# Optimization experiments

Hardware: AMD Instinct MI355X
Metric: run time of the kernel (lower is better)

## Reference

```python
import jax, jax.numpy as jnp
import numpy as np

B, S, D = 2, 2048, 1024
H, Hd = 16, 64
THD = H * Hd  # total_head_dim
LAMBDA_INIT = 0.8
ROPE_BASE = 10000.0
GN_EPS = 1e-5


def _rope_tables(seq_len, head_dim, dtype):
    inv_freq = 1.0 / (ROPE_BASE ** (jnp.arange(0, head_dim, 2, dtype=jnp.float32) / head_dim))
    t = jnp.arange(seq_len, dtype=jnp.float32)
    freqs = jnp.outer(t, inv_freq)                      # (S, Hd/2)
    emb = jnp.concatenate([freqs, freqs], axis=-1)      # (S, Hd)
    return jnp.cos(emb).astype(dtype), jnp.sin(emb).astype(dtype)


def _rotate_half(x):
    x1, x2 = jnp.split(x, 2, axis=-1)
    return jnp.concatenate([-x2, x1], axis=-1)


def _apply_rope(q, k, cos, sin):
    # q, k: (B, H, S, Hd); cos/sin: (S, Hd)
    cos = cos[None, None, :, :]
    sin = sin[None, None, :, :]
    q = q * cos + _rotate_half(q) * sin
    k = k * cos + _rotate_half(k) * sin
    return q, k


def setup_inputs() -> dict:
    key = jax.random.key(0)
    ks = jax.random.split(key, 8)
    s_in = 1.0 / np.sqrt(D)
    s_out = 1.0 / np.sqrt(THD)
    return {
        "x": jax.random.normal(ks[0], (B, S, D), dtype=jnp.float32),
        "Wq": jax.random.normal(ks[1], (D, 2 * THD), dtype=jnp.float32) * s_in,
        "Wk": jax.random.normal(ks[2], (D, 2 * THD), dtype=jnp.float32) * s_in,
        "Wv": jax.random.normal(ks[3], (D, THD), dtype=jnp.float32) * s_in,
        "Wo": jax.random.normal(ks[4], (THD, D), dtype=jnp.float32) * s_out,
        "lambda_q1": jnp.full((H,), LAMBDA_INIT, dtype=jnp.float32),
        "lambda_k1": jnp.full((H,), LAMBDA_INIT, dtype=jnp.float32),
        "lambda_q2": jnp.full((H,), LAMBDA_INIT, dtype=jnp.float32),
        "lambda_k2": jnp.full((H,), LAMBDA_INIT, dtype=jnp.float32),
        "lambda_init": jnp.asarray(LAMBDA_INIT, dtype=jnp.float32),
        "gn_weight": jnp.ones((THD,), dtype=jnp.float32),
        "gn_bias": jnp.zeros((THD,), dtype=jnp.float32),
    }


def reference(x, Wq, Wk, Wv, Wo, lambda_q1, lambda_k1, lambda_q2, lambda_k2,
              lambda_init, gn_weight, gn_bias):
    b, s, _ = x.shape
    scale = Hd ** -0.5

    q = (x @ Wq).reshape(b, s, 2, H, Hd).transpose(0, 2, 3, 1, 4)  # (B,2,H,S,Hd)
    k = (x @ Wk).reshape(b, s, 2, H, Hd).transpose(0, 2, 3, 1, 4)
    v = (x @ Wv).reshape(b, s, H, Hd).transpose(0, 2, 1, 3)        # (B,H,S,Hd)

    q1, q2 = q[:, 0], q[:, 1]
    k1, k2 = k[:, 0], k[:, 1]

    cos, sin = _rope_tables(s, Hd, x.dtype)
    q1, k1 = _apply_rope(q1, k1, cos, sin)
    q2, k2 = _apply_rope(q2, k2, cos, sin)

    attn1 = jax.nn.softmax(jnp.einsum("bhqd,bhkd->bhqk", q1, k1) * scale, axis=-1)
    attn2 = jax.nn.softmax(jnp.einsum("bhqd,bhkd->bhqk", q2, k2) * scale, axis=-1)

    lam1 = jnp.exp(lambda_q1 * lambda_k1).reshape(1, H, 1, 1)
    lam2 = jnp.exp(lambda_q2 * lambda_k2).reshape(1, H, 1, 1)
    lam_full = lam1 - lam2 + lambda_init

    attn_diff = attn1 - lam_full * attn2
    out = jnp.einsum("bhqk,bhkd->bhqd", attn_diff, v)              # (B,H,S,Hd)
    out = out.transpose(0, 2, 1, 3).reshape(b * s, H, Hd)           # (B*S,H,Hd)

    # GroupNorm with num_groups=H over channels THD: normalize each head's Hd
    mean = out.mean(axis=-1, keepdims=True)
    var = out.var(axis=-1, keepdims=True)
    out = (out - mean) * jax.lax.rsqrt(var + GN_EPS)
    out = out * gn_weight.reshape(H, Hd) + gn_bias.reshape(H, Hd)

    out = out.reshape(b, s, THD) * (1.0 - lambda_init)
    return out @ Wo
```

## Files before the change

kernel.cpp:

```cpp
#include <hip/hip_runtime.h>
#include <hip/hip_fp16.h>
#include <math.h>

#define NH     16
#define HD     64
#define S_LEN  2048
#define THD_   1024
#define SCALE_LOG2E 0.18033688011112042f

typedef __fp16 f16x8 __attribute__((ext_vector_type(8)));
typedef __fp16 f16x4 __attribute__((ext_vector_type(4)));
typedef __fp16 f16x2 __attribute__((ext_vector_type(2)));
typedef float  f32x4 __attribute__((ext_vector_type(4)));


__device__ inline void wt_body(const float* __restrict__ W,
                               __half* __restrict__ WT, int id, int nmask,
                               int nshift) {
  int n = id & nmask;
  int k8 = (id >> nshift) * 8;
  int N = nmask + 1;
  f16x8 h;
#pragma unroll
  for (int j = 0; j < 8; ++j)
    h[j] = (__fp16)W[(size_t)(k8 + j) * N + n];
  *(f16x8*)(WT + (size_t)n * 1024 + k8) = h;
}

__global__ __launch_bounds__(256) void prep_kernel(
    const float* __restrict__ Wq, const float* __restrict__ Wk,
    __half* __restrict__ WqT, __half* __restrict__ WkT,
    float2* __restrict__ tab) {
  int bid = blockIdx.x;
  int t = threadIdx.x;
  if (bid < 1024) {
    wt_body(Wq, WqT, bid * 256 + t, 2047, 11);
  } else if (bid < 2048) {
    wt_body(Wk, WkT, (bid - 1024) * 256 + t, 2047, 11);
  } else {
    int id = (bid - 2048) * 256 + t;
    int p = id & 31;
    int s = id >> 5;
    float inv = expf(-0.28782313662425574f * (float)p);
    float sn, cs;
    sincosf((float)s * inv, &sn, &cs);
    tab[id] = make_float2(cs, sn);
  }
}

template <int MODE>
__global__ __launch_bounds__(256) void mfma_gemm(const void* __restrict__ Ap,
                                                 const void* __restrict__ Bp,
                                                 void* __restrict__ Cp,
                                                 const float2* __restrict__ tab) {
  __shared__ __fp16 As[128][72];
  __shared__ __fp16 Bs[64][72];
  const int t = threadIdx.x;
  const int w = t >> 6, lane = t & 63;
  const int quad = lane >> 4, lqi = lane & 15;
  const int wm = w * 32;
  const int n0 = blockIdx.x * 64, m0 = blockIdx.y * 128;

  f32x4 acc[2][4];
#pragma unroll
  for (int mt = 0; mt < 2; ++mt)
#pragma unroll
    for (int nt = 0; nt < 4; ++nt) acc[mt][nt] = (f32x4){0.f, 0.f, 0.f, 0.f};

  const int srow = t >> 3;
  const int sc8 = (t & 7) * 8;
  const int gn_ = t & 63;
  const int gk0 = (t >> 6) * 8;

  for (int k0 = 0; k0 < 1024; k0 += 64) {
    if (k0) __syncthreads();
    if (MODE == 3) {
      const __half* A16 = (const __half*)Ap;
#pragma unroll
      for (int p = 0; p < 4; ++p) {
        int row = srow + 32 * p;
        *(f16x8*)&As[row][sc8] =
            *(const f16x8*)(A16 + (size_t)(m0 + row) * 1024 + k0 + sc8);
      }
    } else {
      const float* A32 = (const float*)Ap;
#pragma unroll
      for (int p = 0; p < 4; ++p) {
        int row = srow + 32 * p;
        const float* src = A32 + (size_t)(m0 + row) * 1024 + k0 + sc8;
        float4 u = *(const float4*)src;
        float4 v = *(const float4*)(src + 4);
        f16x8 h;
        h[0] = (__fp16)u.x; h[1] = (__fp16)u.y;
        h[2] = (__fp16)u.z; h[3] = (__fp16)u.w;
        h[4] = (__fp16)v.x; h[5] = (__fp16)v.y;
        h[6] = (__fp16)v.z; h[7] = (__fp16)v.w;
        *(f16x8*)&As[row][sc8] = h;
      }
    }
    if (MODE == 2) {
      const float* B32 = (const float*)Bp;
#pragma unroll
      for (int p = 0; p < 2; ++p) {
        int kc = gk0 + 32 * p;
        f16x8 h;
#pragma unroll
        for (int j = 0; j < 8; ++j)
          h[j] = (__fp16)B32[(size_t)(k0 + kc + j) * 1024 + n0 + gn_];
        *(f16x8*)&Bs[gn_][kc] = h;
      }
    } else {
      const __half* B16 = (const __half*)Bp;
      if (srow < 32) {
#pragma unroll
        for (int p = 0; p < 2; ++p) {
          int row = srow + 32 * p;
          *(f16x8*)&Bs[row][sc8] =
              *(const f16x8*)(B16 + (size_t)(n0 + row) * 1024 + k0 + sc8);
        }
      }
    }
    __syncthreads();
#pragma unroll
    for (int ks = 0; ks < 2; ++ks) {
      f16x8 af[2], bf[4];
#pragma unroll
      for (int mt = 0; mt < 2; ++mt)
        af[mt] = *(const f16x8*)&As[wm + mt * 16 + lqi][ks * 32 + quad * 8];
#pragma unroll
      for (int nt = 0; nt < 4; ++nt)
        bf[nt] = *(const f16x8*)&Bs[nt * 16 + lqi][ks * 32 + quad * 8];
#pragma unroll
      for (int mt = 0; mt < 2; ++mt)
#pragma unroll
        for (int nt = 0; nt < 4; ++nt)
          acc[mt][nt] = __builtin_amdgcn_mfma_f32_16x16x32_f16(
              af[mt], bf[nt], acc[mt][nt], 0, 0, 0);
    }
  }

  const int b = m0 >> 11;
  const int s0 = (m0 & 2047) + wm + quad * 4;
  if (MODE == 0) {
    __half* dst = (__half*)Cp;
    const int comp = n0 >> 10, hh = (n0 >> 6) & 15;
    __half* base = dst + ((size_t)(b * 2 + comp) * NH + hh) * (size_t)S_LEN * HD;
#pragma unroll
    for (int nt = 0; nt < 2; ++nt) {
      int p = nt * 16 + lqi;
#pragma unroll
      for (int mt = 0; mt < 2; ++mt) {
#pragma unroll
        for (int i = 0; i < 4; ++i) {
          int s = s0 + mt * 16 + i;
          float2 cs = tab[s * 32 + p];
          float x1 = acc[mt][nt][i], x2 = acc[mt][nt + 2][i];
          base[(size_t)s * HD + p] = __float2half(x1 * cs.x - x2 * cs.y);
          base[(size_t)s * HD + p + 32] = __float2half(x2 * cs.x + x1 * cs.y);
        }
      }
    }
  } else if (MODE == 2) {
    __half* vt = (__half*)Cp;
    const int hh = n0 >> 6;
#pragma unroll
    for (int nt = 0; nt < 4; ++nt) {
      int hd = nt * 16 + lqi;
      __half* base = vt + (((size_t)b * NH + hh) * HD + hd) * S_LEN;
#pragma unroll
      for (int mt = 0; mt < 2; ++mt) {
        f16x4 hv;
#pragma unroll
        for (int i = 0; i < 4; ++i) hv[i] = (__fp16)acc[mt][nt][i];
        *(f16x4*)(base + s0 + mt * 16) = hv;
      }
    }
  } else {
    float* Co = (float*)Cp;
#pragma unroll
    for (int mt = 0; mt < 2; ++mt)
#pragma unroll
      for (int i = 0; i < 4; ++i) {
        int m = m0 + wm + mt * 16 + quad * 4 + i;
#pragma unroll
        for (int nt = 0; nt < 4; ++nt)
          Co[(size_t)m * 1024 + n0 + nt * 16 + lqi] = acc[mt][nt][i];
      }
  }
}

__global__ __launch_bounds__(256, 2) void attn_kernel(
    const __half* __restrict__ q_h, const __half* __restrict__ k_h,
    const __half* __restrict__ vt_h, float* __restrict__ out,
    const float* __restrict__ lq1, const float* __restrict__ lk1,
    const float* __restrict__ lq2, const float* __restrict__ lk2,
    const float* __restrict__ lam_init_p) {
  __shared__ __half KV[24][512];
  __shared__ __half P_lds[4][2][32][72];

  const int t = threadIdx.x;
  const int w = t >> 6, lane = t & 63;
  const int quad = lane >> 4, lqi = lane & 15;
  const int qt = blockIdx.x;
  const int bh = blockIdx.y;
  const int b = bh >> 4, h = bh & 15;

  const size_t c1 = ((size_t)(b * 2 + 0) * NH + h) * (size_t)S_LEN * HD;
  const size_t c2 = ((size_t)(b * 2 + 1) * NH + h) * (size_t)S_LEN * HD;
  const size_t vtb = ((size_t)b * NH + h) * (size_t)HD * S_LEN;
  const int q0 = qt * 128 + w * 32;

  f16x8 qf[2][2][2];
#pragma unroll
  for (int nt = 0; nt < 2; ++nt)
#pragma unroll
    for (int ks = 0; ks < 2; ++ks) {
      size_t a = (size_t)(q0 + nt * 16 + lqi) * HD + ks * 32 + quad * 8;
      qf[0][nt][ks] = *(const f16x8*)(q_h + c1 + a);
      qf[1][nt][ks] = *(const f16x8*)(q_h + c2 + a);
    }

  f32x4 O[2][4][2];
#pragma unroll
  for (int s = 0; s < 2; ++s)
#pragma unroll
    for (int mt = 0; mt < 4; ++mt)
#pragma unroll
      for (int nt = 0; nt < 2; ++nt) O[s][mt][nt] = (f32x4){0.f, 0.f, 0.f, 0.f};
  float lsum[2][2] = {{0.f, 0.f}, {0.f, 0.f}};

  auto chunk_addr = [&](int c, int k0) -> const __half* {
    if (c < 16) {
      int str = c >> 3, mt = (c >> 1) & 3, ks = c & 1;
      return k_h + (str ? c2 : c1) + (size_t)(k0 + mt * 16 + lqi) * HD +
             ks * 32 + quad * 8;
    }
    int cc = c - 16, ks2 = cc >> 2, mt = cc & 3;
    return vt_h + vtb + (size_t)(mt * 16 + lqi) * S_LEN + k0 + ks2 * 32 +
           quad * 8;
  };

  f16x8 r[6];
#pragma unroll
  for (int ci = 0; ci < 6; ++ci)
    r[ci] = *(const f16x8*)chunk_addr(w + ci * 4, 0);

  for (int kt = 0; kt < 32; ++kt) {
    if (kt) __syncthreads();
#pragma unroll
    for (int ci = 0; ci < 6; ++ci)
      *(f16x8*)&KV[w + ci * 4][lane * 8] = r[ci];
    __syncthreads();

    if (kt < 31) {
#pragma unroll
      for (int ci = 0; ci < 6; ++ci)
        r[ci] = *(const f16x8*)chunk_addr(w + ci * 4, (kt + 1) * 64);
    }

#pragma unroll
    for (int mt = 0; mt < 4; ++mt) {
#pragma unroll
      for (int str = 0; str < 2; ++str) {
        f16x8 kf0 = *(const f16x8*)&KV[str * 8 + mt * 2 + 0][lane * 8];
        f16x8 kf1 = *(const f16x8*)&KV[str * 8 + mt * 2 + 1][lane * 8];
#pragma unroll
        for (int nt = 0; nt < 2; ++nt) {
          f32x4 s = (f32x4){0.f, 0.f, 0.f, 0.f};
          s = __builtin_amdgcn_mfma_f32_16x16x32_f16(kf0, qf[str][nt][0], s,
                                                     0, 0, 0);
          s = __builtin_amdgcn_mfma_f32_16x16x32_f16(kf1, qf[str][nt][1], s,
                                                     0, 0, 0);
          float e0 = __builtin_amdgcn_exp2f(s[0] * SCALE_LOG2E);
          float e1 = __builtin_amdgcn_exp2f(s[1] * SCALE_LOG2E);
          float e2 = __builtin_amdgcn_exp2f(s[2] * SCALE_LOG2E);
          float e3 = __builtin_amdgcn_exp2f(s[3] * SCALE_LOG2E);
          lsum[str][nt] += (e0 + e1) + (e2 + e3);
          union { f16x4 v; f16x2 h2[2]; } pu;
          pu.h2[0] = __builtin_amdgcn_cvt_pkrtz(e0, e1);
          pu.h2[1] = __builtin_amdgcn_cvt_pkrtz(e2, e3);
          *(f16x4*)&P_lds[w][str][nt * 16 + lqi][mt * 16 + quad * 4] = pu.v;
        }
      }
    }
#pragma unroll
    for (int ks2 = 0; ks2 < 2; ++ks2) {
      f16x8 pf[2][2];
#pragma unroll
      for (int str = 0; str < 2; ++str)
#pragma unroll
        for (int nt = 0; nt < 2; ++nt)
          pf[str][nt] = *(const f16x8*)&P_lds[w][str][nt * 16 + lqi]
                                             [ks2 * 32 + quad * 8];
#pragma unroll
      for (int mt = 0; mt < 4; ++mt) {
        f16x8 vf = *(const f16x8*)&KV[16 + ks2 * 4 + mt][lane * 8];
#pragma unroll
        for (int str = 0; str < 2; ++str)
#pragma unroll
          for (int nt = 0; nt < 2; ++nt)
            O[str][mt][nt] = __builtin_amdgcn_mfma_f32_16x16x32_f16(
                vf, pf[str][nt], O[str][mt][nt], 0, 0, 0);
      }
    }
  }

  const float lam0 = lam_init_p[0];
  const float lam = expf(lq1[h] * lk1[h]) - expf(lq2[h] * lk2[h]) + lam0;
#pragma unroll
  for (int str = 0; str < 2; ++str)
#pragma unroll
    for (int nt = 0; nt < 2; ++nt) {
      float v = lsum[str][nt];
      v += __shfl_xor(v, 16);
      v += __shfl_xor(v, 32);
      lsum[str][nt] = v;
    }
#pragma unroll
  for (int nt = 0; nt < 2; ++nt) {
    float il1 = 1.f / lsum[0][nt];
    float il2 = lam / lsum[1][nt];
    int q = q0 + nt * 16 + lqi;
#pragma unroll
    for (int mt = 0; mt < 4; ++mt) {
      f32x4 o;
#pragma unroll
      for (int i = 0; i < 4; ++i)
        o[i] = O[0][mt][nt][i] * il1 - O[1][mt][nt][i] * il2;
      *(f32x4*)(out + ((size_t)(b * S_LEN + q)) * THD_ + h * HD + mt * 16 +
                quad * 4) = o;
    }
  }
}

__global__ __launch_bounds__(256) void gn_wt_kernel(
    const float* __restrict__ src, __half* __restrict__ dst,
    const float* __restrict__ gw, const float* __restrict__ gb,
    const float* __restrict__ lam_init_p, const float* __restrict__ Wo,
    __half* __restrict__ WoT) {
  if (blockIdx.x >= 16384) {
    wt_body(Wo, WoT, (blockIdx.x - 16384) * 256 + threadIdx.x, 1023, 10);
    return;
  }
  int g = blockIdx.x * 4 + (threadIdx.x >> 6);
  int lane = threadIdx.x & 63;
  float v = src[(size_t)g * 64 + lane];
  float s = v, sq = v * v;
#pragma unroll
  for (int off = 32; off; off >>= 1) {
    s += __shfl_xor(s, off);
    sq += __shfl_xor(sq, off);
  }
  float mean = s * (1.f / 64.f);
  float var = sq * (1.f / 64.f) - mean * mean;
  float rs = rsqrtf(var + 1e-5f);
  int h = g & 15;
  float w = gw[h * 64 + lane], bb = gb[h * 64 + lane];
  dst[(size_t)g * 64 + lane] =
      __float2half(((v - mean) * rs * w + bb) * (1.f - lam_init_p[0]));
}

extern "C" void kernel_launch(void* const* d_in, const int* in_sizes, int n_in,
                              void* d_out, int out_size, void* d_ws,
                              size_t ws_size, hipStream_t stream) {
  const float* x = (const float*)d_in[0];
  const float* Wq = (const float*)d_in[1];
  const float* Wk = (const float*)d_in[2];
  const float* Wv = (const float*)d_in[3];
  const float* Wo = (const float*)d_in[4];
  const float* lq1 = (const float*)d_in[5];
  const float* lk1 = (const float*)d_in[6];
  const float* lq2 = (const float*)d_in[7];
  const float* lk2 = (const float*)d_in[8];
  const float* lam_init = (const float*)d_in[9];
  const float* gnw = (const float*)d_in[10];
  const float* gnb = (const float*)d_in[11];
  float* out = (float*)d_out;

  __half* q_h = (__half*)d_ws;
  __half* k_h = q_h + 8388608;
  __half* vt_h = k_h + 8388608;
  __half* WqT = k_h;
  __half* WkT = vt_h;
  float2* tab = (float2*)(vt_h + 2097152);
  __half* WoT = q_h;
  __half* gn_h = q_h + 1048576;

  dim3 blk(256);
  prep_kernel<<<2304, blk, 0, stream>>>(Wq, Wk, WqT, WkT, tab);
  mfma_gemm<0><<<dim3(32, 32), blk, 0, stream>>>(x, WqT, q_h, tab);
  mfma_gemm<0><<<dim3(32, 32), blk, 0, stream>>>(x, WkT, k_h, tab);
  mfma_gemm<2><<<dim3(16, 32), blk, 0, stream>>>(x, Wv, vt_h, nullptr);
  attn_kernel<<<dim3(16, 32), blk, 0, stream>>>(q_h, k_h, vt_h, out, lq1, lk1,
                                                lq2, lk2, lam_init);
  gn_wt_kernel<<<16896, blk, 0, stream>>>(out, gn_h, gnw, gnb, lam_init, Wo,
                                          WoT);
  mfma_gemm<3><<<dim3(16, 32), blk, 0, stream>>>(gn_h, WoT, out, nullptr);
}
```

Before: 333.2 us.

## Keep softmax probabilities in registers, double-buffer K/V LDS, fold scale into Q

The attention kernel now feeds the exponentiated scores straight from the QK^T MFMA output registers into 16x16x16 MFMAs against V. This removes the per-warp P round trip through shared memory. K/V tiles are double-buffered in LDS with a re-laid-out V buffer, so there is one barrier per tile instead of two. The softmax scale times log2(e) is folded into Q when the Q projection is written, dropping a multiply per score, at the cost of rounding the scaled Q to fp16 and using smaller-K MFMAs.

```diff
diff --git a/kernel.cpp b/kernel.cpp
--- a/kernel.cpp
+++ b/kernel.cpp
@@ -141,7 +141,7 @@
 
   const int b = m0 >> 11;
   const int s0 = (m0 & 2047) + wm + quad * 4;
-  if (MODE == 0) {
+  if (MODE == 0 || MODE == 1) {
     __half* dst = (__half*)Cp;
     const int comp = n0 >> 10, hh = (n0 >> 6) & 15;
     __half* base = dst + ((size_t)(b * 2 + comp) * NH + hh) * (size_t)S_LEN * HD;
@@ -155,8 +155,11 @@
           int s = s0 + mt * 16 + i;
           float2 cs = tab[s * 32 + p];
           float x1 = acc[mt][nt][i], x2 = acc[mt][nt + 2][i];
-          base[(size_t)s * HD + p] = __float2half(x1 * cs.x - x2 * cs.y);
-          base[(size_t)s * HD + p + 32] = __float2half(x2 * cs.x + x1 * cs.y);
+          float y1 = x1 * cs.x - x2 * cs.y;
+          float y2 = x2 * cs.x + x1 * cs.y;
+          if (MODE == 1) { y1 *= SCALE_LOG2E; y2 *= SCALE_LOG2E; }
+          base[(size_t)s * HD + p] = __float2half(y1);
+          base[(size_t)s * HD + p + 32] = __float2half(y2);
         }
       }
     }
@@ -195,8 +198,8 @@
     const float* __restrict__ lq1, const float* __restrict__ lk1,
     const float* __restrict__ lq2, const float* __restrict__ lk2,
     const float* __restrict__ lam_init_p) {
-  __shared__ __half KV[24][512];
-  __shared__ __half P_lds[4][2][32][72];
+  __shared__ __half Ks[2][16][512];
+  __shared__ __half Vs[2][4][64][16];
 
   const int t = threadIdx.x;
   const int w = t >> 6, lane = t & 63;
@@ -224,12 +227,12 @@
 #pragma unroll
   for (int s = 0; s < 2; ++s)
 #pragma unroll
-    for (int mt = 0; mt < 4; ++mt)
-#pragma unroll
-      for (int nt = 0; nt < 2; ++nt) O[s][mt][nt] = (f32x4){0.f, 0.f, 0.f, 0.f};
+    for (int hm = 0; hm < 4; ++hm)
+#pragma unroll
+      for (int nt = 0; nt < 2; ++nt) O[s][hm][nt] = (f32x4){0.f, 0.f, 0.f, 0.f};
   float lsum[2][2] = {{0.f, 0.f}, {0.f, 0.f}};
 
-  auto chunk_addr = [&](int c, int k0) -> const __half* {
+  auto k_src = [&](int c, int k0) -> const __half* {
     if (c < 16) {
       int str = c >> 3, mt = (c >> 1) & 3, ks = c & 1;
       return k_h + (str ? c2 : c1) + (size_t)(k0 + mt * 16 + lqi) * HD +
@@ -239,31 +242,38 @@
     return vt_h + vtb + (size_t)(mt * 16 + lqi) * S_LEN + k0 + ks2 * 32 +
            quad * 8;
   };
+  auto lds_dst = [&](int c, int buf) -> __half* {
+    if (c < 16) return &Ks[buf][c][lane * 8];
+    int cc = c - 16, ks2 = cc >> 2, mt = cc & 3;
+    int kc = ks2 * 2 + (quad >> 1);
+    return &Vs[buf][kc][mt * 16 + lqi][(quad & 1) * 8];
+  };
 
   f16x8 r[6];
 #pragma unroll
-  for (int ci = 0; ci < 6; ++ci)
-    r[ci] = *(const f16x8*)chunk_addr(w + ci * 4, 0);
+  for (int ci = 0; ci < 6; ++ci) r[ci] = *(const f16x8*)k_src(w + ci * 4, 0);
+#pragma unroll
+  for (int ci = 0; ci < 6; ++ci) *(f16x8*)lds_dst(w + ci * 4, 0) = r[ci];
+  __syncthreads();
 
   for (int kt = 0; kt < 32; ++kt) {
-    if (kt) __syncthreads();
-#pragma unroll
-    for (int ci = 0; ci < 6; ++ci)
-      *(f16x8*)&KV[w + ci * 4][lane * 8] = r[ci];
-    __syncthreads();
-
+    const int cur = kt & 1;
     if (kt < 31) {
 #pragma unroll
       for (int ci = 0; ci < 6; ++ci)
-        r[ci] = *(const f16x8*)chunk_addr(w + ci * 4, (kt + 1) * 64);
+        r[ci] = *(const f16x8*)k_src(w + ci * 4, (kt + 1) * 64);
     }
 
 #pragma unroll
     for (int mt = 0; mt < 4; ++mt) {
+      f16x4 vf[4];
+#pragma unroll
+      for (int hm = 0; hm < 4; ++hm)
+        vf[hm] = *(const f16x4*)&Vs[cur][mt][hm * 16 + lqi][quad * 4];
 #pragma unroll
       for (int str = 0; str < 2; ++str) {
-        f16x8 kf0 = *(const f16x8*)&KV[str * 8 + mt * 2 + 0][lane * 8];
-        f16x8 kf1 = *(const f16x8*)&KV[str * 8 + mt * 2 + 1][lane * 8];
+        f16x8 kf0 = *(const f16x8*)&Ks[cur][str * 8 + mt * 2 + 0][lane * 8];
+        f16x8 kf1 = *(const f16x8*)&Ks[cur][str * 8 + mt * 2 + 1][lane * 8];
 #pragma unroll
         for (int nt = 0; nt < 2; ++nt) {
           f32x4 s = (f32x4){0.f, 0.f, 0.f, 0.f};
@@ -271,37 +281,27 @@
                                                      0, 0, 0);
           s = __builtin_amdgcn_mfma_f32_16x16x32_f16(kf1, qf[str][nt][1], s,
                                                      0, 0, 0);
-          float e0 = __builtin_amdgcn_exp2f(s[0] * SCALE_LOG2E);
-          float e1 = __builtin_amdgcn_exp2f(s[1] * SCALE_LOG2E);
-          float e2 = __builtin_amdgcn_exp2f(s[2] * SCALE_LOG2E);
-          float e3 = __builtin_amdgcn_exp2f(s[3] * SCALE_LOG2E);
+          float e0 = __builtin_amdgcn_exp2f(s[0]);
+          float e1 = __builtin_amdgcn_exp2f(s[1]);
+          float e2 = __builtin_amdgcn_exp2f(s[2]);
+          float e3 = __builtin_amdgcn_exp2f(s[3]);
           lsum[str][nt] += (e0 + e1) + (e2 + e3);
           union { f16x4 v; f16x2 h2[2]; } pu;
           pu.h2[0] = __builtin_amdgcn_cvt_pkrtz(e0, e1);
           pu.h2[1] = __builtin_amdgcn_cvt_pkrtz(e2, e3);
-          *(f16x4*)&P_lds[w][str][nt * 16 + lqi][mt * 16 + quad * 4] = pu.v;
+#pragma unroll
+          for (int hm = 0; hm < 4; ++hm)
+            O[str][hm][nt] = __builtin_amdgcn_mfma_f32_16x16x16f16(
+                vf[hm], pu.v, O[str][hm][nt], 0, 0, 0);
         }
       }
     }
-#pragma unroll
-    for (int ks2 = 0; ks2 < 2; ++ks2) {
-      f16x8 pf[2][2];
-#pragma unroll
-      for (int str = 0; str < 2; ++str)
-#pragma unroll
-        for (int nt = 0; nt < 2; ++nt)
-          pf[str][nt] = *(const f16x8*)&P_lds[w][str][nt * 16 + lqi]
-                                             [ks2 * 32 + quad * 8];
-#pragma unroll
-      for (int mt = 0; mt < 4; ++mt) {
-        f16x8 vf = *(const f16x8*)&KV[16 + ks2 * 4 + mt][lane * 8];
-#pragma unroll
-        for (int str = 0; str < 2; ++str)
-#pragma unroll
-          for (int nt = 0; nt < 2; ++nt)
-            O[str][mt][nt] = __builtin_amdgcn_mfma_f32_16x16x32_f16(
-                vf, pf[str][nt], O[str][mt][nt], 0, 0, 0);
-      }
+
+    if (kt < 31) {
+#pragma unroll
+      for (int ci = 0; ci < 6; ++ci)
+        *(f16x8*)lds_dst(w + ci * 4, cur ^ 1) = r[ci];
+      __syncthreads();
     }
   }
 
@@ -322,12 +322,12 @@
     float il2 = lam / lsum[1][nt];
     int q = q0 + nt * 16 + lqi;
 #pragma unroll
-    for (int mt = 0; mt < 4; ++mt) {
+    for (int hm = 0; hm < 4; ++hm) {
       f32x4 o;
 #pragma unroll
       for (int i = 0; i < 4; ++i)
-        o[i] = O[0][mt][nt][i] * il1 - O[1][mt][nt][i] * il2;
-      *(f32x4*)(out + ((size_t)(b * S_LEN + q)) * THD_ + h * HD + mt * 16 +
+        o[i] = O[0][hm][nt][i] * il1 - O[1][hm][nt][i] * il2;
+      *(f32x4*)(out + ((size_t)(b * S_LEN + q)) * THD_ + h * HD + hm * 16 +
                 quad * 4) = o;
     }
   }
@@ -388,7 +388,7 @@
 
   dim3 blk(256);
   prep_kernel<<<2304, blk, 0, stream>>>(Wq, Wk, WqT, WkT, tab);
-  mfma_gemm<0><<<dim3(32, 32), blk, 0, stream>>>(x, WqT, q_h, tab);
+  mfma_gemm<1><<<dim3(32, 32), blk, 0, stream>>>(x, WqT, q_h, tab);
   mfma_gemm<0><<<dim3(32, 32), blk, 0, stream>>>(x, WkT, k_h, tab);
   mfma_gemm<2><<<dim3(16, 32), blk, 0, stream>>>(x, Wv, vt_h, nullptr);
   attn_kernel<<<dim3(16, 32), blk, 0, stream>>>(q_h, k_h, vt_h, out, lq1, lk1,
```

Measured after the change: 363.5 us. 9.1% more time.
